# Optimization experiments

Hardware: AMD Instinct MI355X
Metric: run time of the kernel (lower is better)

Reference implementation:

```python
import jax, jax.numpy as jnp
import numpy as np

B, N, NTYPES, MN = 8, 1024, 2, 128
M = NTYPES * MN
BETA, M1, M2 = 8, 16, 4
NFEAT = M1 * M2
H = 128
NGHOST = 64
RMAX, RMIN = 6.0, 0.5
ENER_SHIFT = np.array([[-93.0], [-13.6]], dtype=np.float32)


def setup_inputs() -> dict:
    key = jax.random.key(0)
    ks = jax.random.split(key, 12)
    # displacement vectors with |r| in (1, Rmax-0.2)
    d = jax.random.normal(ks[0], (B, N, M, 3), jnp.float32)
    d = d / jnp.linalg.norm(d, axis=-1, keepdims=True)
    r = jax.random.uniform(ks[1], (B, N, M, 1), jnp.float32, 1.0, RMAX - 0.2)
    rvec = d * r
    list_neigh = jax.random.randint(ks[2], (B, N, NTYPES, MN), 1, N + NGHOST + 1).astype(jnp.int32)
    # sorted type map so per-type concat order matches original atom order
    Imagetype_map = jnp.concatenate([jnp.zeros(N // 2, jnp.int32), jnp.ones(N - N // 2, jnp.int32)])
    c_param = 0.1 * jax.random.normal(ks[3], (NTYPES, NTYPES, M1, BETA), jnp.float32)
    def w(k, shape):
        fan_in = shape[-2]
        return (1.0 / np.sqrt(fan_in)) * jax.random.normal(k, shape, jnp.float32)
    return {
        'list_neigh': list_neigh,
        'Imagetype_map': Imagetype_map,
        'rvec': rvec,
        'c_param': c_param,
        'W0': w(ks[4], (NTYPES, NFEAT, H)), 'b0': jnp.zeros((NTYPES, H), jnp.float32),
        'W1': w(ks[5], (NTYPES, H, H)),     'b1': jnp.zeros((NTYPES, H), jnp.float32),
        'W2': w(ks[6], (NTYPES, H, H)),     'b2': jnp.zeros((NTYPES, H), jnp.float32),
        'Wout': w(ks[7], (NTYPES, H, 1)),   'bout': jnp.asarray(ENER_SHIFT),
    }


def _cheb(u):
    # Chebyshev polynomials T_0..T_{BETA-1}, stacked on last axis
    Ts = [jnp.ones_like(u), u]
    for _ in range(2, BETA):
        Ts.append(2.0 * u * Ts[-1] - Ts[-2])
    return jnp.stack(Ts[:BETA], axis=-1)


def _features(rvec, Imagetype_map, c_param):
    r = jnp.linalg.norm(rvec, axis=-1)                      # (B,N,M)
    valid = r > 1e-6
    r_safe = jnp.where(valid, r, 1.0)
    span = RMAX - RMIN
    u = jnp.clip(2.0 * (r_safe - RMIN) / span - 1.0, -1.0, 1.0)
    fc = jnp.where(valid & (r_safe < RMAX),
                   0.5 * (jnp.cos(jnp.pi * (jnp.clip(r_safe, RMIN, RMAX) - RMIN) / span) + 1.0),
                   0.0)
    T = _cheb(u)                                            # (B,N,M,BETA)
    # per-pair Chebyshev coefficients c[type_i, type_j, m1, k]; neighbor type is the block index
    c_i = c_param[Imagetype_map]                            # (N, NTYPES, M1, BETA)
    c_pair = jnp.repeat(c_i, MN, axis=1)                    # (N, M, M1, BETA)
    g = jnp.einsum('bnmk,nmpk->bnmp', T, c_pair) * fc[..., None]   # (B,N,M,M1)
    unit = rvec / r_safe[..., None]
    q = jnp.concatenate([jnp.ones_like(r_safe)[..., None], unit], axis=-1)  # (B,N,M,4)
    q = q * valid[..., None]
    S = jnp.einsum('bnmp,bnma->bnpa', g, q) / M             # (B,N,M1,4)
    feat = jnp.einsum('bnpa,bnqa->bnpq', S, S[:, :, :M2])   # (B,N,M1,M2)
    return feat.reshape(feat.shape[0], feat.shape[1], NFEAT)


def _normalize(feat, Imagetype_map):
    # per-type StandardScaler over all feat values of atoms of that type (detached)
    means, stds = [], []
    for t in range(NTYPES):
        w = (Imagetype_map == t).astype(feat.dtype)         # (N,)
        cnt = w.sum() * feat.shape[0] * NFEAT
        mu = (feat * w[None, :, None]).sum() / cnt
        var = (((feat - mu) ** 2) * w[None, :, None]).sum() / (cnt - 1.0)
        means.append(mu)
        stds.append(jnp.sqrt(var))
    means = jax.lax.stop_gradient(jnp.stack(means))
    stds = jax.lax.stop_gradient(jnp.stack(stds))
    mt = means[Imagetype_map][None, :, None]
    st = stds[Imagetype_map][None, :, None]
    return (feat - mt) / st


def _fit(feat_n, Imagetype_map, W0, b0, W1, b1, W2, b2, Wout, bout):
    Ei = jnp.zeros(feat_n.shape[:2] + (1,), feat_n.dtype)
    for t in range(NTYPES):
        h = jnp.tanh(feat_n @ W0[t] + b0[t])
        h = jnp.tanh(h @ W1[t] + b1[t]) + h                 # resnet skip (equal dims)
        h = jnp.tanh(h @ W2[t] + b2[t]) + h
        e = h @ Wout[t] + bout[t]                           # (B,N,1)
        Ei = Ei + e * (Imagetype_map == t)[None, :, None]
    return Ei


def reference(list_neigh, Imagetype_map, rvec, c_param, W0, b0, W1, b1, W2, b2, Wout, bout):
    def ei_fn(rv):
        feat = _features(rv, Imagetype_map, c_param)
        feat_n = _normalize(feat, Imagetype_map)
        return _fit(feat_n, Imagetype_map, W0, b0, W1, b1, W2, b2, Wout, bout)

    Ei = ei_fn(rvec)                                        # (B,N,1)
    Etot = Ei.sum(axis=1)                                   # (B,1)

    # forces / virial: dE/d rij, scatter-add to center & neighbor atoms (incl. ghosts)
    dEdr = jax.grad(lambda rv: ei_fn(rv).sum())(rvec)       # (B,N,M,3)
    Force = jnp.zeros((B, N + NGHOST, 3), rvec.dtype)
    Force = Force.at[:, :N].add(dEdr.sum(axis=2))           # center atoms: F_i = +sum_j dE/drij
    nl = list_neigh.reshape(B, N, M)
    valid = nl > 0
    j = jnp.where(valid, nl - 1, 0)
    flat_idx = (jnp.arange(B)[:, None, None] * (N + NGHOST) + j).reshape(-1)
    contrib = jnp.where(valid[..., None], -dEdr, 0.0).reshape(-1, 3)
    Force = Force.reshape(-1, 3).at[flat_idx].add(contrib).reshape(B, N + NGHOST, 3)
    Virial = -jnp.einsum('bnma,bnmc->bac', rvec, dEdr).reshape(B, 9)
    return (Etot, Ei.squeeze(-1), Force, Virial)
```

## Files before the change

kernel.cpp:

```cpp
#include <hip/hip_runtime.h>
#include <math.h>

#define BB 8
#define NN 1024
#define MM 256
#define BETA 8
#define M1 16
#define NFEAT 64
#define HH 128
#define NTOT 1088
#define F3 (NTOT*3)
#define RMINf 0.5f
#define SPANf 5.5f
#define PIf 3.14159265358979323846f

#define OUT_EI 8
#define OUT_FORCE 8200
#define OUT_VIR 34312

#define MT 16
#define FUSE_BLKS ((BB*NN)/MT)
#define AS0 68
#define AS1 132

#define FEAT_BLKS 2048

#define WS_S     0
#define WS_STATP (WS_S + 8192*64)
#define WS_WTB   (WS_STATP + 8192*2)
#define WS_WB    (WS_WTB + 40960)
#define WT0_OFF  0
#define WT1_OFF  16384
#define WT2_OFF  49152

#define SL_O  0
#define XB_O  1024
#define T0_O  2112
#define H1_O  4224
#define DZ_O  6336
#define CL_O  8448
#define ES_O  8704
#define SRD_O 8720
#define MU_O  8728
#define WR_O  8730
#define VR_O  8922
#define SM_TOT 8958

typedef __attribute__((ext_vector_type(8))) short bf8;
typedef __attribute__((ext_vector_type(4))) float f4;

__device__ __forceinline__ float ftanh(float x) {
  const float e = __expf(2.0f*x);
  return 1.0f - 2.0f/(e + 1.0f);
}
__device__ __forceinline__ short f2bs(float f) {
  unsigned u = __float_as_uint(f);
  return (short)((u + 0x7FFFu + ((u >> 16) & 1u)) >> 16);
}
__device__ __forceinline__ bf8 a_frag(const float* p) {
  bf8 a;
  #pragma unroll
  for (int i = 0; i < 8; ++i) a[i] = f2bs(p[i]);
  return a;
}
__device__ __forceinline__ f4 splat4(float v) {
  f4 r; r[0] = v; r[1] = v; r[2] = v; r[3] = v; return r;
}
__device__ __forceinline__ float dpp_wave_sum(float x) {
  x += __int_as_float(__builtin_amdgcn_update_dpp(0, __float_as_int(x), 0x111, 0xf, 0xf, true));
  x += __int_as_float(__builtin_amdgcn_update_dpp(0, __float_as_int(x), 0x112, 0xf, 0xf, true));
  x += __int_as_float(__builtin_amdgcn_update_dpp(0, __float_as_int(x), 0x114, 0xf, 0xf, true));
  x += __int_as_float(__builtin_amdgcn_update_dpp(0, __float_as_int(x), 0x118, 0xf, 0xf, true));
  x += __int_as_float(__builtin_amdgcn_update_dpp(0, __float_as_int(x), 0x142, 0xf, 0xf, true));
  x += __int_as_float(__builtin_amdgcn_update_dpp(0, __float_as_int(x), 0x143, 0xf, 0xf, true));
  return x;
}

__global__ __launch_bounds__(256) void k_feat(
    const float* __restrict__ rvec, const int* __restrict__ tmap,
    const float* __restrict__ c_param, float* __restrict__ S_ws,
    float* __restrict__ statp,
    const float* __restrict__ W0, const float* __restrict__ W1,
    const float* __restrict__ W2,
    unsigned short* __restrict__ wtb, unsigned short* __restrict__ wb)
{
  const int tid = threadIdx.x;
  if (blockIdx.x >= FEAT_BLKS) {
    const int idx = (blockIdx.x - FEAT_BLKS)*256 + tid;
    if (idx < 81920) {
      unsigned short v;
      if (idx < 16384) {
        const int t = idx >> 13, rem = idx & 8191;
        const int j = rem >> 6, f = rem & 63;
        v = (unsigned short)f2bs(W0[t*8192 + f*128 + j]);
      } else if (idx < 49152) {
        const int i = idx - 16384;
        const int t = i >> 14, rem = i & 16383;
        const int j = rem >> 7, f = rem & 127;
        v = (unsigned short)f2bs(W1[t*16384 + f*128 + j]);
      } else {
        const int i = idx - 49152;
        const int t = i >> 14, rem = i & 16383;
        const int j = rem >> 7, f = rem & 127;
        v = (unsigned short)f2bs(W2[t*16384 + f*128 + j]);
      }
      wtb[idx] = v;
    } else {
      const int k = idx - 81920;
      float src;
      if (k < 16384) src = W0[k];
      else if (k < 49152) src = W1[k - 16384];
      else src = W2[k - 49152];
      wb[k] = (unsigned short)f2bs(src);
    }
    return;
  }
  __shared__ float cA[512];
  __shared__ float Ubuf[4*64];
  __shared__ float Slds[4*64];
  cA[tid] = c_param[tid];
  cA[256 + tid] = c_param[256 + tid];
  __syncthreads();

  const int wave = tid >> 6, lane = tid & 63;
  const int bn = blockIdx.x*4 + wave;
  const int n = bn & (NN-1);
  const int ti = tmap[n];
  const float* rb = rvec + (size_t)bn*MM*3;

  #pragma unroll
  for (int half = 0; half < 2; ++half) {
    float acc[32];
    #pragma unroll
    for (int c = 0; c < 32; ++c) acc[c] = 0.f;
    #pragma unroll
    for (int s = 0; s < 2; ++s) {
      const int m = half*128 + s*64 + lane;
      const float x = rb[3*m], y = rb[3*m+1], z = rb[3*m+2];
      const float r = sqrtf(x*x + y*y + z*z);
      const float ir = 1.0f/r;
      const float ux = x*ir, uy = y*ir, uz = z*ir;
      float u = 2.0f*(r - RMINf)/SPANf - 1.0f;
      u = fminf(fmaxf(u, -1.0f), 1.0f);
      const float fc = 0.5f*(__cosf(PIf*(r - RMINf)/SPANf) + 1.0f);
      float tm2 = 1.0f, tm1 = u;
      acc[0] += fc;  acc[1] += fc*ux;  acc[2] += fc*uy;  acc[3] += fc*uz;
      {
        const float ft = fc*u;
        acc[4] += ft; acc[5] += ft*ux; acc[6] += ft*uy; acc[7] += ft*uz;
      }
      #pragma unroll
      for (int k = 2; k < BETA; ++k) {
        const float tk = 2.0f*u*tm1 - tm2;
        const float ft = fc*tk;
        acc[k*4+0] += ft;
        acc[k*4+1] += ft*ux;
        acc[k*4+2] += ft*uy;
        acc[k*4+3] += ft*uz;
        tm2 = tm1; tm1 = tk;
      }
    }
    #pragma unroll
    for (int c = 0; c < 32; ++c) acc[c] = dpp_wave_sum(acc[c]);
    if (lane == 63) {
      float* Uw = &Ubuf[wave*64 + half*32];
      #pragma unroll
      for (int c = 0; c < 32; ++c) Uw[c] = acc[c];
    }
  }
  {
    const int p = lane >> 2, a = lane & 3;
    const float* Uw = &Ubuf[wave*64];
    const float* cw = &cA[ti*256];
    float s = 0.f;
    #pragma unroll
    for (int tj = 0; tj < 2; ++tj)
      #pragma unroll
      for (int k = 0; k < 8; ++k)
        s += cw[tj*128 + p*8 + k] * Uw[tj*32 + k*4 + a];
    s *= (1.0f/(float)MM);
    Slds[wave*64 + lane] = s;
    S_ws[(size_t)bn*64 + lane] = s;
  }
  {
    const int p = lane >> 2, q = lane & 3;
    const float* Sw = &Slds[wave*64];
    float f = 0.f;
    #pragma unroll
    for (int a = 0; a < 4; ++a) f += Sw[p*4+a]*Sw[q*4+a];
    float fs = f, fss = f*f;
    for (int o = 32; o > 0; o >>= 1) { fs += __shfl_down(fs, o); fss += __shfl_down(fss, o); }
    if (lane == 0) { statp[bn*2+0] = fs; statp[bn*2+1] = fss; }
  }
}

__global__ __launch_bounds__(256, 2) void k_fused(
    const float* __restrict__ S_ws, const int* __restrict__ tmap,
    const float* __restrict__ statp,
    const unsigned short* __restrict__ wtb, const unsigned short* __restrict__ wb,
    const float* __restrict__ b0, const float* __restrict__ b1,
    const float* __restrict__ b2, const float* __restrict__ Wout,
    const float* __restrict__ bout,
    const float* __restrict__ rvec, const int* __restrict__ nlist,
    const float* __restrict__ c_param,
    float* __restrict__ out)
{
  __shared__ float sm[SM_TOT];
  float* sl   = sm + SL_O;
  float* xb   = sm + XB_O;
  float* t0b  = sm + T0_O;
  float* h1b  = sm + H1_O;
  float* dzb  = sm + DZ_O;
  float* c_lds= sm + CL_O;
  float* es   = sm + ES_O;
  float* srd  = sm + SRD_O;
  float* muSd = sm + MU_O;
  float* wredc= sm + WR_O;
  float* vred = sm + VR_O;

  const int tb = blockIdx.x;
  const int bn0 = tb*MT;
  const int b = bn0 >> 10;
  const int n0l = bn0 & (NN-1);
  const int tid = threadIdx.x;
  const int wave = tid >> 6, lane = tid & 63;
  const int quad = lane >> 4, nI = lane & 15;
  const int t = tmap[n0l];
  c_lds[tid] = c_param[t*256 + tid];
  {
    const float4* src = (const float4*)(S_ws + (size_t)bn0*64);
    ((float4*)sl)[tid] = src[tid];
  }
  {
    float fs = 0.f, fss = 0.f;
    #pragma unroll 4
    for (int i = 0; i < 16; ++i) {
      const int e = i*256 + tid;
      const int bb = e >> 9;
      const int n = t*512 + (e & 511);
      const float2 v = *(const float2*)&statp[((size_t)(bb*NN + n))*2];
      fs += v.x; fss += v.y;
    }
    for (int o = 32; o > 0; o >>= 1) { fs += __shfl_down(fs, o); fss += __shfl_down(fss, o); }
    if ((tid & 63) == 0) { srd[(tid>>6)*2] = fs; srd[(tid>>6)*2+1] = fss; }
  }
  __syncthreads();
  if (tid == 0) {
    const float S1 = srd[0]+srd[2]+srd[4]+srd[6];
    const float S2 = srd[1]+srd[3]+srd[5]+srd[7];
    const float cnt = 512.0f * (float)BB * (float)NFEAT;
    const float mu = S1/cnt;
    const float var = (S2 - cnt*mu*mu)/(cnt - 1.0f);
    muSd[0] = mu; muSd[1] = sqrtf(fmaxf(var, 1e-20f));
  }
  __syncthreads();
  const float mu = muSd[0];
  const float inv_sd = 1.0f/muSd[1];
  #pragma unroll
  for (int i = 0; i < 4; ++i) {
    const int e = i*256 + tid;
    const int at = e >> 6, f = e & 63;
    const int p = f >> 2, q = f & 3;
    const float* Sr = &sl[at*64];
    float s = 0.f;
    #pragma unroll
    for (int a = 0; a < 4; ++a) s += Sr[p*4+a]*Sr[q*4+a];
    xb[at*AS0 + f] = (s - mu)*inv_sd;
  }
  __syncthreads();

  const int c0 = (wave*2+0)*16 + nI;
  const int c1 = (wave*2+1)*16 + nI;
  f4 acc0, acc1;

  acc0 = splat4(b0[t*HH + c0]);
  acc1 = splat4(b0[t*HH + c1]);
  {
    const unsigned short* B = wtb + WT0_OFF + t*8192;
    #pragma unroll
    for (int s = 0; s < 2; ++s) {
      const bf8 a  = a_frag(&xb[nI*AS0 + s*32 + quad*8]);
      const bf8 bA = *(const bf8*)&B[(size_t)c0*64 + s*32 + quad*8];
      const bf8 bB = *(const bf8*)&B[(size_t)c1*64 + s*32 + quad*8];
      acc0 = __builtin_amdgcn_mfma_f32_16x16x32_bf16(a, bA, acc0, 0, 0, 0);
      acc1 = __builtin_amdgcn_mfma_f32_16x16x32_bf16(a, bB, acc1, 0, 0, 0);
    }
  }
  #pragma unroll
  for (int r = 0; r < 4; ++r) {
    const int row = quad*4 + r;
    t0b[row*AS1 + c0] = ftanh(acc0[r]);
    t0b[row*AS1 + c1] = ftanh(acc1[r]);
  }
  __syncthreads();
  acc0 = splat4(b1[t*HH + c0]);
  acc1 = splat4(b1[t*HH + c1]);
  {
    const unsigned short* B = wtb + WT1_OFF + t*16384;
    #pragma unroll
    for (int s = 0; s < 4; ++s) {
      const bf8 a  = a_frag(&t0b[nI*AS1 + s*32 + quad*8]);
      const bf8 bA = *(const bf8*)&B[(size_t)c0*128 + s*32 + quad*8];
      const bf8 bB = *(const bf8*)&B[(size_t)c1*128 + s*32 + quad*8];
      acc0 = __builtin_amdgcn_mfma_f32_16x16x32_bf16(a, bA, acc0, 0, 0, 0);
      acc1 = __builtin_amdgcn_mfma_f32_16x16x32_bf16(a, bB, acc1, 0, 0, 0);
    }
  }
  #pragma unroll
  for (int r = 0; r < 4; ++r) {
    const int row = quad*4 + r;
    h1b[row*AS1 + c0] = ftanh(acc0[r]) + t0b[row*AS1 + c0];
    h1b[row*AS1 + c1] = ftanh(acc1[r]) + t0b[row*AS1 + c1];
  }
  __syncthreads();
  acc0 = splat4(b2[t*HH + c0]);
  acc1 = splat4(b2[t*HH + c1]);
  {
    const unsigned short* B = wtb + WT2_OFF + t*16384;
    #pragma unroll
    for (int s = 0; s < 4; ++s) {
      const bf8 a  = a_frag(&h1b[nI*AS1 + s*32 + quad*8]);
      const bf8 bA = *(const bf8*)&B[(size_t)c0*128 + s*32 + quad*8];
      const bf8 bB = *(const bf8*)&B[(size_t)c1*128 + s*32 + quad*8];
      acc0 = __builtin_amdgcn_mfma_f32_16x16x32_bf16(a, bA, acc0, 0, 0, 0);
      acc1 = __builtin_amdgcn_mfma_f32_16x16x32_bf16(a, bB, acc1, 0, 0, 0);
    }
  }
  #pragma unroll
  for (int r = 0; r < 4; ++r) {
    const int row = quad*4 + r;
    dzb[row*AS1 + c0] = acc0[r];
    dzb[row*AS1 + c1] = acc1[r];
  }
  __syncthreads();
  {
    const int at = tid >> 4, cb = (tid & 15)*8;
    const float* wop = Wout + t*HH;
    float ep = 0.f;
    #pragma unroll
    for (int j = 0; j < 8; ++j) {
      const int c = cb + j;
      const float z2 = dzb[at*AS1 + c];
      const float t2 = ftanh(z2);
      const float wo = wop[c];
      ep += (t2 + h1b[at*AS1 + c])*wo;
      dzb[at*AS1 + c] = wo*(1.0f - t2*t2);
    }
    ep += __shfl_down(ep, 8, 16);
    ep += __shfl_down(ep, 4, 16);
    ep += __shfl_down(ep, 2, 16);
    ep += __shfl_down(ep, 1, 16);
    if ((tid & 15) == 0) es[at] = ep;
  }
  __syncthreads();
  if (tid < MT) out[OUT_EI + bn0 + tid] = es[tid] + bout[t];
  if (tid == 0) {
    float s = 0.f;
    #pragma unroll
    for (int i = 0; i < MT; ++i) s += es[i];
    atomicAdd(&out[b], s + (float)MT*bout[t]);
  }

  {
    const float* wop = Wout + t*HH;
    acc0 = splat4(wop[c0]);
    acc1 = splat4(wop[c1]);
    const unsigned short* B = wb + WT2_OFF + t*16384;
    #pragma unroll
    for (int s = 0; s < 4; ++s) {
      const bf8 a  = a_frag(&dzb[nI*AS1 + s*32 + quad*8]);
      const bf8 bA = *(const bf8*)&B[(size_t)c0*128 + s*32 + quad*8];
      const bf8 bB = *(const bf8*)&B[(size_t)c1*128 + s*32 + quad*8];
      acc0 = __builtin_amdgcn_mfma_f32_16x16x32_bf16(a, bA, acc0, 0, 0, 0);
      acc1 = __builtin_amdgcn_mfma_f32_16x16x32_bf16(a, bB, acc1, 0, 0, 0);
    }
  }
  __syncthreads();
  float dh10[4], dh11[4];
  #pragma unroll
  for (int r = 0; r < 4; ++r) {
    const int row = quad*4 + r;
    dh10[r] = acc0[r]; dh11[r] = acc1[r];
    const float t1a = h1b[row*AS1 + c0] - t0b[row*AS1 + c0];
    const float t1b = h1b[row*AS1 + c1] - t0b[row*AS1 + c1];
    dzb[row*AS1 + c0] = acc0[r]*(1.0f - t1a*t1a);
    dzb[row*AS1 + c1] = acc1[r]*(1.0f - t1b*t1b);
  }
  __syncthreads();
  acc0[0]=dh10[0]; acc0[1]=dh10[1]; acc0[2]=dh10[2]; acc0[3]=dh10[3];
  acc1[0]=dh11[0]; acc1[1]=dh11[1]; acc1[2]=dh11[2]; acc1[3]=dh11[3];
  {
    const unsigned short* B = wb + WT1_OFF + t*16384;
    #pragma unroll
    for (int s = 0; s < 4; ++s) {
      const bf8 a  = a_frag(&dzb[nI*AS1 + s*32 + quad*8]);
      const bf8 bA = *(const bf8*)&B[(size_t)c0*128 + s*32 + quad*8];
      const bf8 bB = *(const bf8*)&B[(size_t)c1*128 + s*32 + quad*8];
      acc0 = __builtin_amdgcn_mfma_f32_16x16x32_bf16(a, bA, acc0, 0, 0, 0);
      acc1 = __builtin_amdgcn_mfma_f32_16x16x32_bf16(a, bB, acc1, 0, 0, 0);
    }
  }
  __syncthreads();
  #pragma unroll
  for (int r = 0; r < 4; ++r) {
    const int row = quad*4 + r;
    const float ta = t0b[row*AS1 + c0], tb2 = t0b[row*AS1 + c1];
    dzb[row*AS1 + c0] = acc0[r]*(1.0f - ta*ta);
    dzb[row*AS1 + c1] = acc1[r]*(1.0f - tb2*tb2);
  }
  __syncthreads();
  {
    const int cx = wave*16 + nI;
    acc0 = splat4(0.f);
    const unsigned short* B = wb + WT0_OFF + t*8192;
    #pragma unroll
    for (int s = 0; s < 4; ++s) {
      const bf8 a  = a_frag(&dzb[nI*AS1 + s*32 + quad*8]);
      const bf8 bA = *(const bf8*)&B[(size_t)cx*128 + s*32 + quad*8];
      acc0 = __builtin_amdgcn_mfma_f32_16x16x32_bf16(a, bA, acc0, 0, 0, 0);
    }
    __syncthreads();
    float* Db = dzb;
    #pragma unroll
    for (int r = 0; r < 4; ++r)
      Db[(quad*4 + r)*64 + cx] = acc0[r]*inv_sd;
  }
  __syncthreads();

  {
    float* dSb = t0b;
    const float* Db = dzb;
    #pragma unroll
    for (int it = 0; it < 4; ++it) {
      const int idx = it*256 + tid;
      const int at = idx >> 6, f = idx & 63;
      const int i = f >> 2, a = f & 3;
      const float* Sr = &sl[at*64];
      const float* Dr = &Db[at*64];
      float v = 0.f;
      #pragma unroll
      for (int q = 0; q < 4; ++q) v += Dr[i*4+q]*Sr[q*4+a];
      if (i < 4)
        for (int p = 0; p < 16; ++p) v += Dr[p*4+i]*Sr[p*4+a];
      dSb[idx] = v;
    }
  }
  __syncthreads();
  {
    float* Eb = h1b;
    const float* dSb = t0b;
    #pragma unroll
    for (int it = 0; it < 4; ++it) {
      const int idx = it*256 + tid;
      const int at = idx >> 6, rem = idx & 63;
      const int tj = rem >> 5, a = (rem >> 3) & 3, k = rem & 7;
      float e = 0.f;
      #pragma unroll
      for (int p = 0; p < 16; ++p) e += dSb[at*64 + p*4 + a]*c_lds[tj*128 + p*8 + k];
      Eb[idx] = e;
    }
  }
  __syncthreads();
  {
    const float4 z4 = {0.f, 0.f, 0.f, 0.f};
    for (int i = tid; i < F3/4; i += 256) ((float4*)sm)[i] = z4;
  }
  __syncthreads();

  float* fpart = sm;
  const float* Eb = h1b;
  float vir[9];
  #pragma unroll
  for (int i = 0; i < 9; ++i) vir[i] = 0.f;
  const int tjm = tid >> 7;
  const float dudr = 2.0f/SPANf;
  const float invM = 1.0f/(float)MM;

  const size_t rowbase = (size_t)bn0*MM;
  float px0, py0, pz0, px1, py1, pz1; int pnl0, pnl1;
  {
    const float* rp0 = rvec + (rowbase + tid)*3;
    const float* rp1 = rvec + (rowbase + MM + tid)*3;
    px0 = rp0[0]; py0 = rp0[1]; pz0 = rp0[2]; pnl0 = nlist[rowbase + tid];
    px1 = rp1[0]; py1 = rp1[1]; pz1 = rp1[2]; pnl1 = nlist[rowbase + MM + tid];
  }
  for (int a0 = 0; a0 < MT; a0 += 2) {
    const float x0 = px0, y0 = py0, z0 = pz0; const int nl0 = pnl0;
    const float x1 = px1, y1 = py1, z1 = pz1; const int nl1 = pnl1;
    if (a0 + 2 < MT) {
      const float* rp0 = rvec + (rowbase + (size_t)(a0+2)*MM + tid)*3;
      const float* rp1 = rvec + (rowbase + (size_t)(a0+3)*MM + tid)*3;
      px0 = rp0[0]; py0 = rp0[1]; pz0 = rp0[2];
      pnl0 = nlist[rowbase + (size_t)(a0+2)*MM + tid];
      px1 = rp1[0]; py1 = rp1[1]; pz1 = rp1[2];
      pnl1 = nlist[rowbase + (size_t)(a0+3)*MM + tid];
    }
    float Er0[32], Er1[32];
    {
      const float4* p0 = (const float4*)&Eb[a0*64 + tjm*32];
      const float4* p1 = (const float4*)&Eb[(a0+1)*64 + tjm*32];
      #pragma unroll
      for (int q = 0; q < 8; ++q) {
        const float4 v0 = p0[q], v1 = p1[q];
        Er0[q*4+0]=v0.x; Er0[q*4+1]=v0.y; Er0[q*4+2]=v0.z; Er0[q*4+3]=v0.w;
        Er1[q*4+0]=v1.x; Er1[q*4+1]=v1.y; Er1[q*4+2]=v1.z; Er1[q*4+3]=v1.w;
      }
    }
    const float r_0 = sqrtf(x0*x0 + y0*y0 + z0*z0);
    const float r_1 = sqrtf(x1*x1 + y1*y1 + z1*z1);
    const float ir0 = 1.0f/r_0, ir1 = 1.0f/r_1;
    const float ux0 = x0*ir0, uy0 = y0*ir0, uz0 = z0*ir0;
    const float ux1 = x1*ir1, uy1 = y1*ir1, uz1 = z1*ir1;
    float u0 = 2.0f*(r_0 - RMINf)/SPANf - 1.0f;
    float u1 = 2.0f*(r_1 - RMINf)/SPANf - 1.0f;
    u0 = fminf(fmaxf(u0, -1.0f), 1.0f);
    u1 = fminf(fmaxf(u1, -1.0f), 1.0f);
    float s0a, c0a, s1a, c1a;
    __sincosf(PIf*(r_0 - RMINf)/SPANf, &s0a, &c0a);
    __sincosf(PIf*(r_1 - RMINf)/SPANf, &s1a, &c1a);
    const float fc0 = 0.5f*(c0a + 1.0f), dfc0 = -0.5f*(PIf/SPANf)*s0a;
    const float fc1 = 0.5f*(c1a + 1.0f), dfc1 = -0.5f*(PIf/SPANf)*s1a;
    float ta0[4], tda0[4], ta1[4], tda1[4];
    #pragma unroll
    for (int aa = 0; aa < 4; ++aa) {
      ta0[aa]  = Er0[aa*8] + Er0[aa*8+1]*u0;
      tda0[aa] = Er0[aa*8+1];
      ta1[aa]  = Er1[aa*8] + Er1[aa*8+1]*u1;
      tda1[aa] = Er1[aa*8+1];
    }
    float t0m2 = 1.f, t0m1 = u0, d0m2 = 0.f, d0m1 = 1.f;
    float t1m2 = 1.f, t1m1 = u1, d1m2 = 0.f, d1m1 = 1.f;
    #pragma unroll
    for (int k = 2; k < BETA; ++k) {
      const float tk0 = 2.f*u0*t0m1 - t0m2;
      const float dk0 = 2.f*t0m1 + 2.f*u0*d0m1 - d0m2;
      const float tk1 = 2.f*u1*t1m1 - t1m2;
      const float dk1 = 2.f*t1m1 + 2.f*u1*d1m1 - d1m2;
      #pragma unroll
      for (int aa = 0; aa < 4; ++aa) {
        ta0[aa]  += Er0[aa*8+k]*tk0;
        tda0[aa] += Er0[aa*8+k]*dk0;
        ta1[aa]  += Er1[aa*8+k]*tk1;
        tda1[aa] += Er1[aa*8+k]*dk1;
      }
      t0m2 = t0m1; t0m1 = tk0; d0m2 = d0m1; d0m1 = dk0;
      t1m2 = t1m1; t1m1 = tk1; d1m2 = d1m1; d1m1 = dk1;
    }
    float A0 = dfc0*(ta0[0] + ux0*ta0[1] + uy0*ta0[2] + uz0*ta0[3])
             + fc0*dudr*(tda0[0] + ux0*tda0[1] + uy0*tda0[2] + uz0*tda0[3]);
    float A1 = dfc1*(ta1[0] + ux1*ta1[1] + uy1*ta1[2] + uz1*ta1[3])
             + fc1*dudr*(tda1[0] + ux1*tda1[1] + uy1*tda1[2] + uz1*tda1[3]);
    float q10 = fc0*ta0[1], q20 = fc0*ta0[2], q30 = fc0*ta0[3];
    float q11 = fc1*ta1[1], q21 = fc1*ta1[2], q31 = fc1*ta1[3];
    A0 *= invM; q10 *= invM; q20 *= invM; q30 *= invM;
    A1 *= invM; q11 *= invM; q21 *= invM; q31 *= invM;
    const float qu0 = q10*ux0 + q20*uy0 + q30*uz0;
    const float qu1 = q11*ux1 + q21*uy1 + q31*uz1;
    const float d00 = A0*ux0 + (q10 - qu0*ux0)*ir0;
    const float d01 = A0*uy0 + (q20 - qu0*uy0)*ir0;
    const float d02 = A0*uz0 + (q30 - qu0*uz0)*ir0;
    const float d10 = A1*ux1 + (q11 - qu1*ux1)*ir1;
    const float d11 = A1*uy1 + (q21 - qu1*uy1)*ir1;
    const float d12 = A1*uz1 + (q31 - qu1*uz1)*ir1;
    if (nl0 > 0) {
      const int j = nl0 - 1;
      atomicAdd(&fpart[j*3+0], -d00);
      atomicAdd(&fpart[j*3+1], -d01);
      atomicAdd(&fpart[j*3+2], -d02);
    }
    if (nl1 > 0) {
      const int j = nl1 - 1;
      atomicAdd(&fpart[j*3+0], -d10);
      atomicAdd(&fpart[j*3+1], -d11);
      atomicAdd(&fpart[j*3+2], -d12);
    }
    vir[0] -= x0*d00 + x1*d10; vir[1] -= x0*d01 + x1*d11; vir[2] -= x0*d02 + x1*d12;
    vir[3] -= y0*d00 + y1*d10; vir[4] -= y0*d01 + y1*d11; vir[5] -= y0*d02 + y1*d12;
    vir[6] -= z0*d00 + z1*d10; vir[7] -= z0*d01 + z1*d11; vir[8] -= z0*d02 + z1*d12;
    const float r00 = dpp_wave_sum(d00), r01 = dpp_wave_sum(d01), r02 = dpp_wave_sum(d02);
    const float r10 = dpp_wave_sum(d10), r11 = dpp_wave_sum(d11), r12 = dpp_wave_sum(d12);
    if (lane == 63) {
      wredc[(a0*4 + wave)*3 + 0] = r00;
      wredc[(a0*4 + wave)*3 + 1] = r01;
      wredc[(a0*4 + wave)*3 + 2] = r02;
      wredc[((a0+1)*4 + wave)*3 + 0] = r10;
      wredc[((a0+1)*4 + wave)*3 + 1] = r11;
      wredc[((a0+1)*4 + wave)*3 + 2] = r12;
    }
  }
  #pragma unroll
  for (int i = 0; i < 9; ++i) {
    const float v = dpp_wave_sum(vir[i]);
    if (lane == 63) vred[wave*9 + i] = v;
  }
  __syncthreads();
  if (tid < MT*3) {
    const int at = tid/3, c = tid - at*3;
    const float v = wredc[(at*4+0)*3+c] + wredc[(at*4+1)*3+c]
                  + wredc[(at*4+2)*3+c] + wredc[(at*4+3)*3+c];
    atomicAdd(&fpart[(n0l+at)*3 + c], v);
  }
  if (tid >= 64 && tid < 73) {
    const int i = tid - 64;
    atomicAdd(&out[OUT_VIR + b*9 + i],
              vred[i] + vred[9+i] + vred[18+i] + vred[27+i]);
  }
  __syncthreads();
  {
    float* dst = out + OUT_FORCE + (size_t)b*F3;
    for (int i = tid; i < F3; i += 256)
      atomicAdd(&dst[i], fpart[i]);
  }
}

extern "C" void kernel_launch(void* const* d_in, const int* in_sizes, int n_in,
                              void* d_out, int out_size, void* d_ws, size_t ws_size,
                              hipStream_t stream)
{
  const int*   nlist = (const int*)d_in[0];
  const int*   tmap  = (const int*)d_in[1];
  const float* rvec  = (const float*)d_in[2];
  const float* cpar  = (const float*)d_in[3];
  const float* W0 = (const float*)d_in[4];
  const float* b0 = (const float*)d_in[5];
  const float* W1 = (const float*)d_in[6];
  const float* b1 = (const float*)d_in[7];
  const float* W2 = (const float*)d_in[8];
  const float* b2 = (const float*)d_in[9];
  const float* Wout = (const float*)d_in[10];
  const float* bout = (const float*)d_in[11];
  float* out = (float*)d_out;
  float* ws = (float*)d_ws;
  float* S_ws   = ws + WS_S;
  float* statp  = ws + WS_STATP;
  unsigned short* wtb = (unsigned short*)(ws + WS_WTB);
  unsigned short* wb  = (unsigned short*)(ws + WS_WB);

  hipMemsetAsync(d_out, 0, (size_t)out_size, stream);

  k_feat <<<FEAT_BLKS + 640, 256, 0, stream>>>(rvec, tmap, cpar, S_ws, statp,
                                               W0, W1, W2, wtb, wb);
  k_fused<<<FUSE_BLKS, 256, 0, stream>>>(S_ws, tmap, statp, wtb, wb,
                                         b0, b1, b2, Wout, bout,
                                         rvec, nlist, cpar, out);
}
```

Before: 168.0 us.

## Merge feature and fused kernels into one cooperative kernel with grid sync

Replaces the memset, feature kernel and fused MLP/force kernel with a single cooperative kernel. Each block computes its 16 atoms' descriptors straight into shared memory, writes per-block normalization partials, zeroes the output and converts weights, then does a grid-wide sync before normalization and the rest. This removes the S workspace round trip and two launch boundaries. The cost is a grid barrier across 512 blocks that needs every block co-resident, and each wave now processes four atoms serially in the feature phase with lower parallelism. The weight-to-bf16 conversion still runs each call.

```diff
diff --git a/kernel.cpp b/kernel.cpp
--- a/kernel.cpp
+++ b/kernel.cpp
@@ -1,5 +1,8 @@
 #include <hip/hip_runtime.h>
+#include <hip/hip_cooperative_groups.h>
 #include <math.h>
+
+namespace cg = cooperative_groups;
 
 #define BB 8
 #define NN 1024
@@ -17,18 +20,16 @@
 #define OUT_EI 8
 #define OUT_FORCE 8200
 #define OUT_VIR 34312
+#define OUT_TOT (OUT_VIR + BB*9)
 
 #define MT 16
 #define FUSE_BLKS ((BB*NN)/MT)
 #define AS0 68
 #define AS1 132
 
-#define FEAT_BLKS 2048
-
-#define WS_S     0
-#define WS_STATP (WS_S + 8192*64)
-#define WS_WTB   (WS_STATP + 8192*2)
-#define WS_WB    (WS_WTB + 40960)
+#define WS_WTB   0
+#define WS_WB    40960
+#define WS_BSTAT 81920
 #define WT0_OFF  0
 #define WT1_OFF  16384
 #define WT2_OFF  49152
@@ -76,134 +77,15 @@
   return x;
 }
 
-__global__ __launch_bounds__(256) void k_feat(
-    const float* __restrict__ rvec, const int* __restrict__ tmap,
-    const float* __restrict__ c_param, float* __restrict__ S_ws,
-    float* __restrict__ statp,
+__global__ __launch_bounds__(256, 2) void k_mega(
+    const float* __restrict__ rvec, const int* __restrict__ nlist,
+    const int* __restrict__ tmap, const float* __restrict__ c_param,
     const float* __restrict__ W0, const float* __restrict__ W1,
-    const float* __restrict__ W2,
-    unsigned short* __restrict__ wtb, unsigned short* __restrict__ wb)
-{
-  const int tid = threadIdx.x;
-  if (blockIdx.x >= FEAT_BLKS) {
-    const int idx = (blockIdx.x - FEAT_BLKS)*256 + tid;
-    if (idx < 81920) {
-      unsigned short v;
-      if (idx < 16384) {
-        const int t = idx >> 13, rem = idx & 8191;
-        const int j = rem >> 6, f = rem & 63;
-        v = (unsigned short)f2bs(W0[t*8192 + f*128 + j]);
-      } else if (idx < 49152) {
-        const int i = idx - 16384;
-        const int t = i >> 14, rem = i & 16383;
-        const int j = rem >> 7, f = rem & 127;
-        v = (unsigned short)f2bs(W1[t*16384 + f*128 + j]);
-      } else {
-        const int i = idx - 49152;
-        const int t = i >> 14, rem = i & 16383;
-        const int j = rem >> 7, f = rem & 127;
-        v = (unsigned short)f2bs(W2[t*16384 + f*128 + j]);
-      }
-      wtb[idx] = v;
-    } else {
-      const int k = idx - 81920;
-      float src;
-      if (k < 16384) src = W0[k];
-      else if (k < 49152) src = W1[k - 16384];
-      else src = W2[k - 49152];
-      wb[k] = (unsigned short)f2bs(src);
-    }
-    return;
-  }
-  __shared__ float cA[512];
-  __shared__ float Ubuf[4*64];
-  __shared__ float Slds[4*64];
-  cA[tid] = c_param[tid];
-  cA[256 + tid] = c_param[256 + tid];
-  __syncthreads();
-
-  const int wave = tid >> 6, lane = tid & 63;
-  const int bn = blockIdx.x*4 + wave;
-  const int n = bn & (NN-1);
-  const int ti = tmap[n];
-  const float* rb = rvec + (size_t)bn*MM*3;
-
-  #pragma unroll
-  for (int half = 0; half < 2; ++half) {
-    float acc[32];
-    #pragma unroll
-    for (int c = 0; c < 32; ++c) acc[c] = 0.f;
-    #pragma unroll
-    for (int s = 0; s < 2; ++s) {
-      const int m = half*128 + s*64 + lane;
-      const float x = rb[3*m], y = rb[3*m+1], z = rb[3*m+2];
-      const float r = sqrtf(x*x + y*y + z*z);
-      const float ir = 1.0f/r;
-      const float ux = x*ir, uy = y*ir, uz = z*ir;
-      float u = 2.0f*(r - RMINf)/SPANf - 1.0f;
-      u = fminf(fmaxf(u, -1.0f), 1.0f);
-      const float fc = 0.5f*(__cosf(PIf*(r - RMINf)/SPANf) + 1.0f);
-      float tm2 = 1.0f, tm1 = u;
-      acc[0] += fc;  acc[1] += fc*ux;  acc[2] += fc*uy;  acc[3] += fc*uz;
-      {
-        const float ft = fc*u;
-        acc[4] += ft; acc[5] += ft*ux; acc[6] += ft*uy; acc[7] += ft*uz;
-      }
-      #pragma unroll
-      for (int k = 2; k < BETA; ++k) {
-        const float tk = 2.0f*u*tm1 - tm2;
-        const float ft = fc*tk;
-        acc[k*4+0] += ft;
-        acc[k*4+1] += ft*ux;
-        acc[k*4+2] += ft*uy;
-        acc[k*4+3] += ft*uz;
-        tm2 = tm1; tm1 = tk;
-      }
-    }
-    #pragma unroll
-    for (int c = 0; c < 32; ++c) acc[c] = dpp_wave_sum(acc[c]);
-    if (lane == 63) {
-      float* Uw = &Ubuf[wave*64 + half*32];
-      #pragma unroll
-      for (int c = 0; c < 32; ++c) Uw[c] = acc[c];
-    }
-  }
-  {
-    const int p = lane >> 2, a = lane & 3;
-    const float* Uw = &Ubuf[wave*64];
-    const float* cw = &cA[ti*256];
-    float s = 0.f;
-    #pragma unroll
-    for (int tj = 0; tj < 2; ++tj)
-      #pragma unroll
-      for (int k = 0; k < 8; ++k)
-        s += cw[tj*128 + p*8 + k] * Uw[tj*32 + k*4 + a];
-    s *= (1.0f/(float)MM);
-    Slds[wave*64 + lane] = s;
-    S_ws[(size_t)bn*64 + lane] = s;
-  }
-  {
-    const int p = lane >> 2, q = lane & 3;
-    const float* Sw = &Slds[wave*64];
-    float f = 0.f;
-    #pragma unroll
-    for (int a = 0; a < 4; ++a) f += Sw[p*4+a]*Sw[q*4+a];
-    float fs = f, fss = f*f;
-    for (int o = 32; o > 0; o >>= 1) { fs += __shfl_down(fs, o); fss += __shfl_down(fss, o); }
-    if (lane == 0) { statp[bn*2+0] = fs; statp[bn*2+1] = fss; }
-  }
-}
-
-__global__ __launch_bounds__(256, 2) void k_fused(
-    const float* __restrict__ S_ws, const int* __restrict__ tmap,
-    const float* __restrict__ statp,
-    const unsigned short* __restrict__ wtb, const unsigned short* __restrict__ wb,
-    const float* __restrict__ b0, const float* __restrict__ b1,
-    const float* __restrict__ b2, const float* __restrict__ Wout,
-    const float* __restrict__ bout,
-    const float* __restrict__ rvec, const int* __restrict__ nlist,
-    const float* __restrict__ c_param,
-    float* __restrict__ out)
+    const float* __restrict__ W2, const float* __restrict__ b0,
+    const float* __restrict__ b1, const float* __restrict__ b2,
+    const float* __restrict__ Wout, const float* __restrict__ bout,
+    unsigned short* __restrict__ wtb, unsigned short* __restrict__ wb,
+    float* __restrict__ bstat, float* __restrict__ out)
 {
   __shared__ float sm[SM_TOT];
   float* sl   = sm + SL_O;
@@ -226,23 +108,132 @@
   const int wave = tid >> 6, lane = tid & 63;
   const int quad = lane >> 4, nI = lane & 15;
   const int t = tmap[n0l];
+  const int gid = tb*256 + tid;
+
+  for (int i = gid; i < OUT_TOT; i += FUSE_BLKS*256) out[i] = 0.f;
+
+  for (int idx = gid; idx < 163840; idx += FUSE_BLKS*256) {
+    if (idx < 81920) {
+      unsigned short v;
+      if (idx < 16384) {
+        const int tt = idx >> 13, rem = idx & 8191;
+        const int j = rem >> 6, f = rem & 63;
+        v = (unsigned short)f2bs(W0[tt*8192 + f*128 + j]);
+      } else if (idx < 49152) {
+        const int i2 = idx - 16384;
+        const int tt = i2 >> 14, rem = i2 & 16383;
+        const int j = rem >> 7, f = rem & 127;
+        v = (unsigned short)f2bs(W1[tt*16384 + f*128 + j]);
+      } else {
+        const int i2 = idx - 49152;
+        const int tt = i2 >> 14, rem = i2 & 16383;
+        const int j = rem >> 7, f = rem & 127;
+        v = (unsigned short)f2bs(W2[tt*16384 + f*128 + j]);
+      }
+      wtb[idx] = v;
+    } else {
+      const int k = idx - 81920;
+      float src;
+      if (k < 16384) src = W0[k];
+      else if (k < 49152) src = W1[k - 16384];
+      else src = W2[k - 49152];
+      wb[k] = (unsigned short)f2bs(src);
+    }
+  }
+
   c_lds[tid] = c_param[t*256 + tid];
-  {
-    const float4* src = (const float4*)(S_ws + (size_t)bn0*64);
-    ((float4*)sl)[tid] = src[tid];
-  }
+
+  {
+    float* Ubuf = t0b;
+    float* afs  = wredc;
+    float* afss = wredc + 16;
+    const float invM = 1.0f/(float)MM;
+    for (int a = 0; a < 4; ++a) {
+      const int at = wave*4 + a;
+      const float* rb = rvec + (size_t)(bn0 + at)*MM*3;
+      #pragma unroll
+      for (int half = 0; half < 2; ++half) {
+        float acc[32];
+        #pragma unroll
+        for (int c = 0; c < 32; ++c) acc[c] = 0.f;
+        #pragma unroll
+        for (int s = 0; s < 2; ++s) {
+          const int m = half*128 + s*64 + lane;
+          const float x = rb[3*m], y = rb[3*m+1], z = rb[3*m+2];
+          const float r = sqrtf(x*x + y*y + z*z);
+          const float ir = 1.0f/r;
+          const float ux = x*ir, uy = y*ir, uz = z*ir;
+          float u = 2.0f*(r - RMINf)/SPANf - 1.0f;
+          u = fminf(fmaxf(u, -1.0f), 1.0f);
+          const float fc = 0.5f*(__cosf(PIf*(r - RMINf)/SPANf) + 1.0f);
+          float tm2 = 1.0f, tm1 = u;
+          acc[0] += fc;  acc[1] += fc*ux;  acc[2] += fc*uy;  acc[3] += fc*uz;
+          {
+            const float ft = fc*u;
+            acc[4] += ft; acc[5] += ft*ux; acc[6] += ft*uy; acc[7] += ft*uz;
+          }
+          #pragma unroll
+          for (int k = 2; k < BETA; ++k) {
+            const float tk = 2.0f*u*tm1 - tm2;
+            const float ft = fc*tk;
+            acc[k*4+0] += ft;
+            acc[k*4+1] += ft*ux;
+            acc[k*4+2] += ft*uy;
+            acc[k*4+3] += ft*uz;
+            tm2 = tm1; tm1 = tk;
+          }
+        }
+        #pragma unroll
+        for (int c = 0; c < 32; ++c) acc[c] = dpp_wave_sum(acc[c]);
+        if (lane == 63) {
+          float* Uw = &Ubuf[wave*64 + half*32];
+          #pragma unroll
+          for (int c = 0; c < 32; ++c) Uw[c] = acc[c];
+        }
+      }
+      {
+        const int p = lane >> 2, a4 = lane & 3;
+        const float* Uw = &Ubuf[wave*64];
+        const float* cw = c_lds;
+        float s = 0.f;
+        #pragma unroll
+        for (int tj = 0; tj < 2; ++tj)
+          #pragma unroll
+          for (int k = 0; k < 8; ++k)
+            s += cw[tj*128 + p*8 + k] * Uw[tj*32 + k*4 + a4];
+        s *= invM;
+        sl[at*64 + lane] = s;
+      }
+      {
+        const int p = lane >> 2, q = lane & 3;
+        const float* Sw = &sl[at*64];
+        float f = 0.f;
+        #pragma unroll
+        for (int a4 = 0; a4 < 4; ++a4) f += Sw[p*4+a4]*Sw[q*4+a4];
+        float fs = f, fss = f*f;
+        for (int o = 32; o > 0; o >>= 1) { fs += __shfl_down(fs, o); fss += __shfl_down(fss, o); }
+        if (lane == 0) { afs[at] = fs; afss[at] = fss; }
+      }
+    }
+    __syncthreads();
+    if (tid == 0) {
+      float s1 = 0.f, s2 = 0.f;
+      #pragma unroll
+      for (int i = 0; i < MT; ++i) { s1 += afs[i]; s2 += afss[i]; }
+      bstat[tb*2+0] = s1; bstat[tb*2+1] = s2;
+    }
+  }
+  __threadfence();
+  cg::this_grid().sync();
+
   {
     float fs = 0.f, fss = 0.f;
-    #pragma unroll 4
-    for (int i = 0; i < 16; ++i) {
-      const int e = i*256 + tid;
-      const int bb = e >> 9;
-      const int n = t*512 + (e & 511);
-      const float2 v = *(const float2*)&statp[((size_t)(bb*NN + n))*2];
-      fs += v.x; fss += v.y;
+    for (int j = tid; j < FUSE_BLKS; j += 256) {
+      const int jt = tmap[(j*MT) & (NN-1)];
+      if (jt == t) { fs += bstat[j*2]; fss += bstat[j*2+1]; }
     }
     for (int o = 32; o > 0; o >>= 1) { fs += __shfl_down(fs, o); fss += __shfl_down(fss, o); }
-    if ((tid & 63) == 0) { srd[(tid>>6)*2] = fs; srd[(tid>>6)*2+1] = fss; }
+    if (lane == 0) { srd[wave*2] = fs; srd[wave*2+1] = fss; }
   }
   __syncthreads();
   if (tid == 0) {
@@ -631,16 +622,15 @@
   const float* bout = (const float*)d_in[11];
   float* out = (float*)d_out;
   float* ws = (float*)d_ws;
-  float* S_ws   = ws + WS_S;
-  float* statp  = ws + WS_STATP;
   unsigned short* wtb = (unsigned short*)(ws + WS_WTB);
   unsigned short* wb  = (unsigned short*)(ws + WS_WB);
-
-  hipMemsetAsync(d_out, 0, (size_t)out_size, stream);
-
-  k_feat <<<FEAT_BLKS + 640, 256, 0, stream>>>(rvec, tmap, cpar, S_ws, statp,
-                                               W0, W1, W2, wtb, wb);
-  k_fused<<<FUSE_BLKS, 256, 0, stream>>>(S_ws, tmap, statp, wtb, wb,
-                                         b0, b1, b2, Wout, bout,
-                                         rvec, nlist, cpar, out);
+  float* bstat = ws + WS_BSTAT;
+
+  void* kargs[] = { (void*)&rvec, (void*)&nlist, (void*)&tmap, (void*)&cpar,
+                    (void*)&W0, (void*)&W1, (void*)&W2,
+                    (void*)&b0, (void*)&b1, (void*)&b2,
+                    (void*)&Wout, (void*)&bout,
+                    (void*)&wtb, (void*)&wb, (void*)&bstat, (void*)&out };
+  hipLaunchCooperativeKernel((void*)k_mega, dim3(FUSE_BLKS), dim3(256),
+                             kargs, 0, stream);
 }
```

Measured after the change: 271.8 us. 1.62x slower.
